# Kernel tuning notes

Measured on AMD Instinct MI355X. Metric: run time of the kernel, lower is better.

## Reference

```python
import jax, jax.numpy as jnp
from jax import lax
import numpy as np

B, S, H, DIN, BIN, NH, NL = 32, 256, 256, 16, 2, 8, 3
DH = H // NH


def setup_inputs() -> dict:
    key = jax.random.key(0)
    it = iter(jax.random.split(key, 40))
    def nrm(shape, s=0.05):
        return jax.random.normal(next(it), shape, jnp.float32) * s
    return {
        "parts": jax.random.normal(next(it), (B, S, DIN), jnp.float32),
        "bin_info": jax.random.normal(next(it), (B, BIN), jnp.float32),
        "target": jax.random.randint(next(it), (B, S), 0, S, dtype=jnp.int32),
        "pe_W1": nrm((H // 2, DIN)), "pe_b1": jnp.zeros((H // 2,), jnp.float32),
        "pe_W2": nrm((H // 2, H // 2)), "pe_b2": jnp.zeros((H // 2,), jnp.float32),
        "be_W1": nrm((H // 4, BIN)), "be_b1": jnp.zeros((H // 4,), jnp.float32),
        "be_W2": nrm((H // 4, H // 4)), "be_b2": jnp.zeros((H // 4,), jnp.float32),
        "pos_emb": nrm((S, H // 4)),
        "tr_Wqkv": nrm((NL, 3 * H, H)), "tr_bqkv": jnp.zeros((NL, 3 * H), jnp.float32),
        "tr_Wo": nrm((NL, H, H)), "tr_bo": jnp.zeros((NL, H), jnp.float32),
        "tr_ln1_g": jnp.ones((NL, H), jnp.float32), "tr_ln1_b": jnp.zeros((NL, H), jnp.float32),
        "tr_ff_W1": nrm((NL, 2 * H, H)), "tr_ff_b1": jnp.zeros((NL, 2 * H), jnp.float32),
        "tr_ff_W2": nrm((NL, H, 2 * H)), "tr_ff_b2": jnp.zeros((NL, H), jnp.float32),
        "tr_ln2_g": jnp.ones((NL, H), jnp.float32), "tr_ln2_b": jnp.zeros((NL, H), jnp.float32),
        "lstm_Wih": nrm((4 * H, H)), "lstm_Whh": nrm((4 * H, H)),
        "lstm_bih": jnp.zeros((4 * H,), jnp.float32), "lstm_bhh": jnp.zeros((4 * H,), jnp.float32),
        "ptr_W": nrm((H, H)), "ptr_b": jnp.zeros((H,), jnp.float32),
        "ptr_v": nrm((H,)),
    }


def _ln(x, g, b):
    m = x.mean(-1, keepdims=True)
    v = ((x - m) ** 2).mean(-1, keepdims=True)
    return (x - m) / jnp.sqrt(v + 1e-5) * g + b


def _forward(parts, bin_info, target, pe_W1, pe_b1, pe_W2, pe_b2,
             be_W1, be_b1, be_W2, be_b2, pos_emb,
             tr_Wqkv, tr_bqkv, tr_Wo, tr_bo, tr_ln1_g, tr_ln1_b,
             tr_ff_W1, tr_ff_b1, tr_ff_W2, tr_ff_b2, tr_ln2_g, tr_ln2_b,
             lstm_Wih, lstm_Whh, lstm_bih, lstm_bhh, ptr_W, ptr_b, ptr_v):
    # --- encode_inputs (dropout inactive in eval) ---
    p = jax.nn.relu(parts @ pe_W1.T + pe_b1) @ pe_W2.T + pe_b2            # [B,S,H/2]
    bb = jax.nn.relu(bin_info @ be_W1.T + be_b1) @ be_W2.T + be_b2        # [B,H/4]
    bb = jnp.broadcast_to(bb[:, None, :], (B, S, H // 4))
    pe = jnp.broadcast_to(pos_emb[None], (B, S, H // 4))
    x = jnp.concatenate([p, bb, pe], axis=-1)                             # [B,S,H]
    scale = 1.0 / np.sqrt(DH)
    for l in range(NL):  # post-norm TransformerEncoderLayer, relu FFN
        qkv = x @ tr_Wqkv[l].T + tr_bqkv[l]
        q, k, v = jnp.split(qkv, 3, axis=-1)
        q = q.reshape(B, S, NH, DH).transpose(0, 2, 1, 3)
        k = k.reshape(B, S, NH, DH).transpose(0, 2, 1, 3)
        v = v.reshape(B, S, NH, DH).transpose(0, 2, 1, 3)
        a = jax.nn.softmax(jnp.einsum('bhqd,bhkd->bhqk', q, k) * scale, axis=-1)
        o = jnp.einsum('bhqk,bhkd->bhqd', a, v).transpose(0, 2, 1, 3).reshape(B, S, H)
        x = _ln(x + o @ tr_Wo[l].T + tr_bo[l], tr_ln1_g[l], tr_ln1_b[l])
        ff = jax.nn.relu(x @ tr_ff_W1[l].T + tr_ff_b1[l]) @ tr_ff_W2[l].T + tr_ff_b2[l]
        x = _ln(x + ff, tr_ln2_g[l], tr_ln2_b[l])
    enc = x
    # Note: the original's inner MultiheadAttention calls never feed the
    # returned step_logits (part_logit is overwritten), so the faithful output is
    # logits[b,t,i] = v . tanh(ptr(h_t) + ptr(enc_i)), vectorized over i here.
    e_proj = enc @ ptr_W.T + ptr_b                                        # [B,S,H]
    bidx = jnp.arange(B)

    def step(carry, tgt_t):
        h, c, xin = carry
        g = xin @ lstm_Wih.T + lstm_bih + h @ lstm_Whh.T + lstm_bhh
        i, f, gg, o = jnp.split(g, 4, axis=-1)
        c = jax.nn.sigmoid(f) * c + jax.nn.sigmoid(i) * jnp.tanh(gg)
        h = jax.nn.sigmoid(o) * jnp.tanh(c)
        hp = h @ ptr_W.T + ptr_b                                          # [B,H]
        logits = jnp.tanh(hp[:, None, :] + e_proj) @ ptr_v                # [B,S]
        nxt = enc[bidx, tgt_t]                                            # teacher forcing
        return (h, c, nxt), logits

    z = jnp.zeros((B, H), jnp.float32)
    _, logits = lax.scan(step, (z, z, z), target.T)                       # [S,B,S]
    return logits.transpose(1, 0, 2)                                      # [B,S,S]


def reference(parts, bin_info, target, pe_W1, pe_b1, pe_W2, pe_b2,
              be_W1, be_b1, be_W2, be_b2, pos_emb,
              tr_Wqkv, tr_bqkv, tr_Wo, tr_bo, tr_ln1_g, tr_ln1_b,
              tr_ff_W1, tr_ff_b1, tr_ff_W2, tr_ff_b2, tr_ln2_g, tr_ln2_b,
              lstm_Wih, lstm_Whh, lstm_bih, lstm_bhh, ptr_W, ptr_b, ptr_v):
    return _forward(parts, bin_info, target, pe_W1, pe_b1, pe_W2, pe_b2,
                    be_W1, be_b1, be_W2, be_b2, pos_emb,
                    tr_Wqkv, tr_bqkv, tr_Wo, tr_bo, tr_ln1_g, tr_ln1_b,
                    tr_ff_W1, tr_ff_b1, tr_ff_W2, tr_ff_b2, tr_ln2_g, tr_ln2_b,
                    lstm_Wih, lstm_Whh, lstm_bih, lstm_bhh, ptr_W, ptr_b, ptr_v)
```

## Files before the change

kernel.cpp:

```cpp
#include <hip/hip_runtime.h>
#include <cstddef>

#define DEV __device__ __forceinline__

DEV float fexp2(float x) { return __builtin_amdgcn_exp2f(x); }
DEV float frcp(float x)  { return __builtin_amdgcn_rcpf(x); }
DEV float fsigm(float x) { return frcp(1.0f + fexp2(-1.44269504f * x)); }
DEV float ftanh_(float x){ return 1.0f - 2.0f * frcp(1.0f + fexp2(2.88539008f * x)); }

typedef _Float16 h2t __attribute__((ext_vector_type(2)));
typedef _Float16 v8h __attribute__((ext_vector_type(8)));
typedef float v4f __attribute__((ext_vector_type(4)));
union U32H2 { unsigned int u; h2t h; };
DEV h2t u2h(unsigned int u) { U32H2 x; x.u = u; return x.h; }

template <int BM, int BN, bool RELU, bool OUTF16>
__global__ __launch_bounds__(256) void hgemm_kernel(
    const _Float16* __restrict__ A, const _Float16* __restrict__ W,
    const float* __restrict__ bias1, const float* __restrict__ bias2,
    void* __restrict__ Cout, int M, int N, int K)
{
    constexpr int MT = BM / 32;
    constexpr int NT = BN / 32;
    constexpr int RA = BM / 64;
    constexpr int RB = BN / 64;
    __shared__ _Float16 As[BM * 32];
    __shared__ _Float16 Bs[BN * 32];

    const int tid = threadIdx.x;
    const int lane = tid & 63;
    const int lm = lane & 15, lq = lane >> 4;
    const int wrow = ((tid >> 6) & 1) * (BM / 2);
    const int wcol = (tid >> 7) * (BN / 2);
    const int m0 = blockIdx.x * BM, n0 = blockIdx.y * BN;
    const _Float16* Ab = A + (size_t)m0 * K;
    const _Float16* Wb = W + (size_t)n0 * K;

    v4f acc[MT][NT];
#pragma unroll
    for (int i = 0; i < MT; ++i)
#pragma unroll
        for (int j = 0; j < NT; ++j) acc[i][j] = (v4f){0.f, 0.f, 0.f, 0.f};

    const int rowS = tid >> 2, qS = tid & 3;

    uint4 ra[RA], rb[RB];
#pragma unroll
    for (int r = 0; r < RA; ++r)
        ra[r] = *(const uint4*)(Ab + (size_t)(rowS + 64 * r) * K + qS * 8);
#pragma unroll
    for (int r = 0; r < RB; ++r)
        rb[r] = *(const uint4*)(Wb + (size_t)(rowS + 64 * r) * K + qS * 8);

    for (int k0 = 0; k0 < K; k0 += 32) {
        __syncthreads();
#pragma unroll
        for (int r = 0; r < RA; ++r)
            *(uint4*)(As + (size_t)(tid + 256 * r) * 8) = ra[r];
#pragma unroll
        for (int r = 0; r < RB; ++r)
            *(uint4*)(Bs + (size_t)(tid + 256 * r) * 8) = rb[r];
        __syncthreads();
        int kn = k0 + 32;
        if (kn < K) {
#pragma unroll
            for (int r = 0; r < RA; ++r)
                ra[r] = *(const uint4*)(Ab + (size_t)(rowS + 64 * r) * K + kn + qS * 8);
#pragma unroll
            for (int r = 0; r < RB; ++r)
                rb[r] = *(const uint4*)(Wb + (size_t)(rowS + 64 * r) * K + kn + qS * 8);
        }
        v8h af[MT], bf[NT];
#pragma unroll
        for (int i = 0; i < MT; ++i)
            af[i] = *(const v8h*)(As + (size_t)(wrow + i * 16 + lm) * 32 + lq * 8);
#pragma unroll
        for (int j = 0; j < NT; ++j)
            bf[j] = *(const v8h*)(Bs + (size_t)(wcol + j * 16 + lm) * 32 + lq * 8);
#pragma unroll
        for (int i = 0; i < MT; ++i)
#pragma unroll
            for (int j = 0; j < NT; ++j)
                acc[i][j] = __builtin_amdgcn_mfma_f32_16x16x32_f16(
                    af[i], bf[j], acc[i][j], 0, 0, 0);
    }

#pragma unroll
    for (int j = 0; j < NT; ++j) {
        int col = n0 + wcol + j * 16 + lm;
        float bv = bias1[col];
        if (bias2) bv += bias2[col];
#pragma unroll
        for (int i = 0; i < MT; ++i) {
            int rbase = m0 + wrow + i * 16 + lq * 4;
#pragma unroll
            for (int rg = 0; rg < 4; ++rg) {
                float vv = acc[i][j][rg] + bv;
                if (RELU) vv = fmaxf(vv, 0.f);
                if (OUTF16)
                    ((_Float16*)Cout)[(size_t)(rbase + rg) * N + col] = (_Float16)vv;
                else
                    ((float*)Cout)[(size_t)(rbase + rg) * N + col] = vv;
            }
        }
    }
}

__global__ __launch_bounds__(256) void hgemm_ln_kernel(
    const _Float16* __restrict__ A, const _Float16* __restrict__ W,
    const float* __restrict__ bias, const float* __restrict__ gamma,
    const float* __restrict__ beta, float* __restrict__ X,
    _Float16* __restrict__ X16, int K)
{
    constexpr int BM = 64, BN = 256, MT = 2, NT = 8, RA = 1, RB = 4;
    __shared__ _Float16 As[BM * 32];
    __shared__ _Float16 Bs[BN * 32];
    __shared__ float redS[2][BM][2];

    const int tid = threadIdx.x;
    const int lane = tid & 63;
    const int lm = lane & 15, lq = lane >> 4;
    const int wrow = ((tid >> 6) & 1) * 32;
    const int wcol = (tid >> 7) * 128;
    const int half = tid >> 7;
    const int m0 = blockIdx.x * BM;
    const _Float16* Ab = A + (size_t)m0 * K;

    v4f acc[MT][NT];
#pragma unroll
    for (int i = 0; i < MT; ++i)
#pragma unroll
        for (int j = 0; j < NT; ++j) acc[i][j] = (v4f){0.f, 0.f, 0.f, 0.f};

    const int rowS = tid >> 2, qS = tid & 3;

    uint4 ra[RA], rb[RB];
#pragma unroll
    for (int r = 0; r < RA; ++r)
        ra[r] = *(const uint4*)(Ab + (size_t)(rowS + 64 * r) * K + qS * 8);
#pragma unroll
    for (int r = 0; r < RB; ++r)
        rb[r] = *(const uint4*)(W + (size_t)(rowS + 64 * r) * K + qS * 8);

    for (int k0 = 0; k0 < K; k0 += 32) {
        __syncthreads();
#pragma unroll
        for (int r = 0; r < RA; ++r)
            *(uint4*)(As + (size_t)(tid + 256 * r) * 8) = ra[r];
#pragma unroll
        for (int r = 0; r < RB; ++r)
            *(uint4*)(Bs + (size_t)(tid + 256 * r) * 8) = rb[r];
        __syncthreads();
        int kn = k0 + 32;
        if (kn < K) {
#pragma unroll
            for (int r = 0; r < RA; ++r)
                ra[r] = *(const uint4*)(Ab + (size_t)(rowS + 64 * r) * K + kn + qS * 8);
#pragma unroll
            for (int r = 0; r < RB; ++r)
                rb[r] = *(const uint4*)(W + (size_t)(rowS + 64 * r) * K + kn + qS * 8);
        }
        v8h af[MT], bf[NT];
#pragma unroll
        for (int i = 0; i < MT; ++i)
            af[i] = *(const v8h*)(As + (size_t)(wrow + i * 16 + lm) * 32 + lq * 8);
#pragma unroll
        for (int j = 0; j < NT; ++j)
            bf[j] = *(const v8h*)(Bs + (size_t)(wcol + j * 16 + lm) * 32 + lq * 8);
#pragma unroll
        for (int i = 0; i < MT; ++i)
#pragma unroll
            for (int j = 0; j < NT; ++j)
                acc[i][j] = __builtin_amdgcn_mfma_f32_16x16x32_f16(
                    af[i], bf[j], acc[i][j], 0, 0, 0);
    }

    float s[MT][4], s2[MT][4];
#pragma unroll
    for (int i = 0; i < MT; ++i)
#pragma unroll
        for (int rg = 0; rg < 4; ++rg) { s[i][rg] = 0.f; s2[i][rg] = 0.f; }
#pragma unroll
    for (int j = 0; j < NT; ++j) {
        int col = wcol + j * 16 + lm;
        float bv = bias[col];
#pragma unroll
        for (int i = 0; i < MT; ++i) {
            int rbase = m0 + wrow + i * 16 + lq * 4;
#pragma unroll
            for (int rg = 0; rg < 4; ++rg) {
                float y = acc[i][j][rg] + bv + X[(size_t)(rbase + rg) * 256 + col];
                acc[i][j][rg] = y;
                s[i][rg] += y;
                s2[i][rg] += y * y;
            }
        }
    }
#pragma unroll
    for (int i = 0; i < MT; ++i)
#pragma unroll
        for (int rg = 0; rg < 4; ++rg) {
            float a = s[i][rg], b2 = s2[i][rg];
#pragma unroll
            for (int m = 1; m < 16; m <<= 1) {
                a += __shfl_xor(a, m);
                b2 += __shfl_xor(b2, m);
            }
            if (lm == 0) {
                int rloc = wrow + i * 16 + lq * 4 + rg;
                redS[half][rloc][0] = a;
                redS[half][rloc][1] = b2;
            }
        }
    __syncthreads();
#pragma unroll
    for (int i = 0; i < MT; ++i) {
#pragma unroll
        for (int rg = 0; rg < 4; ++rg) {
            int rloc = wrow + i * 16 + lq * 4 + rg;
            float st = redS[0][rloc][0] + redS[1][rloc][0];
            float s2t = redS[0][rloc][1] + redS[1][rloc][1];
            float mean = st * (1.f / 256.f);
            float var = s2t * (1.f / 256.f) - mean * mean;
            float inv = rsqrtf(var + 1e-5f);
            size_t rowb = (size_t)(m0 + rloc) * 256;
#pragma unroll
            for (int j = 0; j < NT; ++j) {
                int col = wcol + j * 16 + lm;
                float o = (acc[i][j][rg] - mean) * inv * gamma[col] + beta[col];
                X[rowb + col] = o;
                X16[rowb + col] = (_Float16)o;
            }
        }
    }
}

__global__ __launch_bounds__(256) void cvt_fused_kernel(
    const float* __restrict__ s0, const float* __restrict__ s1,
    const float* __restrict__ s2, const float* __restrict__ s3,
    const float* __restrict__ s4, const float* __restrict__ s5,
    _Float16* __restrict__ dst,
    const float* __restrict__ Whh, unsigned int* __restrict__ WB,
    const float* __restrict__ bih, const float* __restrict__ bhh,
    float* __restrict__ PB)
{
    if (blockIdx.x < 7424) {
        int i = blockIdx.x * 256 + threadIdx.x;
        if (i >= 1900544) return;
        float val;
        if (i < 589824)       val = s0[i];
        else if (i < 786432)  val = s1[i - 589824];
        else if (i < 1179648) val = s2[i - 786432];
        else if (i < 1572864) val = s3[i - 1179648];
        else if (i < 1835008) {
            int idx = i - 1572864;
            int rp = idx >> 8, k = idx & 255;
            int j = rp >> 2, g = rp & 3;
            val = s4[(g * 256 + j) * 256 + k];
        }
        else                  val = s5[i - 1835008];
        dst[i] = (_Float16)val;
    } else {
        int idx = (blockIdx.x - 7424) * 256 + threadIdx.x;
        if (idx < 1024) {
            int j = idx >> 2, g = idx & 3;
            PB[idx] = bih[g * 256 + j] + bhh[g * 256 + j];
        }
        int l = idx & 3;
        int gt = idx >> 2;
        int tid = gt & 511;
        int q = gt >> 9;
        int i, c;
        if (q < 8)       { i = q >> 1; c = q & 1; }
        else if (q < 52) { int qq = q - 8; i = qq / 11; c = 2 + qq % 11; }
        else if (q < 56) { i = q - 52; c = 13; }
        else if (q < 58) { i = q - 56; c = 14; }
        else if (q < 60) { i = 2 + (q - 58); c = 14; }
        else             { i = q - 60; c = 15; }
        int r = ((tid & 255) << 2) + i;
        int k = ((tid >> 8) << 7) + (c << 3) + (l << 1);
        _Float16 lo = (_Float16)Whh[r * 256 + k];
        _Float16 hi = (_Float16)Whh[r * 256 + k + 1];
        U32H2 x; x.h = h2t{lo, hi};
        WB[idx] = x.u;
    }
}

__global__ __launch_bounds__(128) void part_enc_kernel(
    const float* __restrict__ parts, const float* __restrict__ W1,
    const float* __restrict__ b1, const float* __restrict__ W2,
    const float* __restrict__ b2, const float* __restrict__ bin_info,
    const float* __restrict__ be_W1, const float* __restrict__ be_b1,
    const float* __restrict__ be_W2, const float* __restrict__ be_b2,
    const float* __restrict__ pos_emb, float* __restrict__ X,
    _Float16* __restrict__ X16)
{
    __shared__ float W2s[128][129];
    __shared__ float h1[128];
    __shared__ float pin[16];
    __shared__ float h1b[64];
    __shared__ float bb_s[64];
    int tid = threadIdx.x;
    int b = blockIdx.x >> 3, s0 = (blockIdx.x & 7) * 32;
    for (int l = 0; l < 128; ++l) W2s[l][tid] = W2[l * 128 + tid];
    {
        float x0 = bin_info[b * 2], x1 = bin_info[b * 2 + 1];
        if (tid < 64)
            h1b[tid] = fmaxf(be_W1[tid * 2] * x0 + be_W1[tid * 2 + 1] * x1
                             + be_b1[tid], 0.f);
        __syncthreads();
        if (tid < 64) {
            float a = be_b2[tid];
#pragma unroll 4
            for (int e = 0; e < 64; ++e) a += be_W2[tid * 64 + e] * h1b[e];
            bb_s[tid] = a;
        }
        __syncthreads();
    }
    float w1r[16];
#pragma unroll
    for (int k = 0; k < 16; ++k) w1r[k] = W1[tid * 16 + k];
    float bias1v = b1[tid], bias2v = b2[tid];
    for (int si = 0; si < 32; ++si) {
        int s = s0 + si;
        size_t row = (size_t)b * 256 + s;
        if (tid < 16) pin[tid] = parts[row * 16 + tid];
        __syncthreads();
        float h = bias1v;
#pragma unroll
        for (int k = 0; k < 16; ++k) h += w1r[k] * pin[k];
        h1[tid] = fmaxf(h, 0.f);
        __syncthreads();
        float acc = bias2v;
#pragma unroll 4
        for (int e = 0; e < 128; ++e) acc += W2s[tid][e] * h1[e];
        X[row * 256 + tid] = acc;
        X16[row * 256 + tid] = (_Float16)acc;
        if (tid < 64) {
            float bbv = bb_s[tid];
            float pev = pos_emb[s * 64 + tid];
            X[row * 256 + 128 + tid] = bbv;
            X[row * 256 + 192 + tid] = pev;
            X16[row * 256 + 128 + tid] = (_Float16)bbv;
            X16[row * 256 + 192 + tid] = (_Float16)pev;
        }
        __syncthreads();
    }
}

__global__ __launch_bounds__(256) void attn_mfma_kernel(
    const _Float16* __restrict__ QKV, _Float16* __restrict__ O16)
{
    int bh = blockIdx.x;
    int b = bh >> 3, h = bh & 7;
    const int tid = threadIdx.x;
    const int w = tid >> 6;
    const int lane = tid & 63;
    const int lm = lane & 15, lq = lane >> 4;
    const float c_se = 0.17677669529663687f * 1.44269504f;

    __shared__ _Float16 Ks[4][256][8];
    __shared__ _Float16 Vt[32][264];
    __shared__ _Float16 Ps[4][16][264];

    const _Float16* qkvb = QKV + (size_t)(b * 256) * 768 + h * 32;
    {
        int s = tid;
        const _Float16* kr = qkvb + (size_t)s * 768 + 256;
#pragma unroll
        for (int c = 0; c < 4; ++c)
            *(uint4*)&Ks[c][s][0] = *(const uint4*)(kr + c * 8);
        const _Float16* vr = qkvb + (size_t)s * 768 + 512;
        _Float16 vtmp[32];
        *(uint4*)&vtmp[0]  = *(const uint4*)(vr);
        *(uint4*)&vtmp[8]  = *(const uint4*)(vr + 8);
        *(uint4*)&vtmp[16] = *(const uint4*)(vr + 16);
        *(uint4*)&vtmp[24] = *(const uint4*)(vr + 24);
#pragma unroll
        for (int d = 0; d < 32; ++d) Vt[d][s] = vtmp[d];
    }
    __syncthreads();

#pragma unroll 1
    for (int st = 0; st < 4; ++st) {
        int rt = w * 4 + st;
        v8h qf = *(const v8h*)(QKV + (size_t)(b * 256 + rt * 16 + lm) * 768
                               + h * 32 + lq * 8);
        v4f acc[16];
#pragma unroll
        for (int ct = 0; ct < 16; ++ct) {
            v8h kf = *(const v8h*)&Ks[lq][ct * 16 + lm][0];
            acc[ct] = __builtin_amdgcn_mfma_f32_16x16x32_f16(
                qf, kf, (v4f){0.f, 0.f, 0.f, 0.f}, 0, 0, 0);
        }
        float sminv[4];
#pragma unroll
        for (int r = 0; r < 4; ++r) {
            float m = acc[0][r];
#pragma unroll
            for (int ct = 1; ct < 16; ++ct) m = fmaxf(m, acc[ct][r]);
#pragma unroll
            for (int msk = 1; msk < 16; msk <<= 1)
                m = fmaxf(m, __shfl_xor(m, msk));
            float ssum = 0.f;
#pragma unroll
            for (int ct = 0; ct < 16; ++ct) {
                float e = fexp2((acc[ct][r] - m) * c_se);
                acc[ct][r] = e;
                ssum += e;
            }
#pragma unroll
            for (int msk = 1; msk < 16; msk <<= 1)
                ssum += __shfl_xor(ssum, msk);
            sminv[r] = frcp(ssum);
        }
#pragma unroll
        for (int ct = 0; ct < 16; ++ct)
#pragma unroll
            for (int r = 0; r < 4; ++r)
                Ps[w][lq * 4 + r][ct * 16 + lm] =
                    (_Float16)(acc[ct][r] * sminv[r]);
#pragma unroll
        for (int dt = 0; dt < 2; ++dt) {
            v4f o = (v4f){0.f, 0.f, 0.f, 0.f};
#pragma unroll
            for (int jc = 0; jc < 8; ++jc) {
                v8h pf = *(const v8h*)&Ps[w][lm][jc * 32 + lq * 8];
                v8h vf = *(const v8h*)&Vt[dt * 16 + lm][jc * 32 + lq * 8];
                o = __builtin_amdgcn_mfma_f32_16x16x32_f16(pf, vf, o, 0, 0, 0);
            }
#pragma unroll
            for (int r = 0; r < 4; ++r)
                O16[(size_t)(b * 256 + rt * 16 + lq * 4 + r) * 256
                    + h * 32 + dt * 16 + lm] = (_Float16)o[r];
        }
    }
}

__global__ __launch_bounds__(256) void gather_kernel(
    const float* __restrict__ X, const int* __restrict__ target,
    _Float16* __restrict__ Xg16)
{
    int row = blockIdx.x;
    int b = row >> 8, t = row & 255;
    int d = threadIdx.x;
    float val = 0.f;
    if (t > 0) {
        int src = target[b * 256 + t - 1];
        val = X[((size_t)b * 256 + src) * 256 + d];
    }
    Xg16[(size_t)row * 256 + d] = (_Float16)val;
}

__global__ __launch_bounds__(512) void lstm_kernel(
    const _Float16* __restrict__ g_in, const uint4* __restrict__ WB4,
    _Float16* __restrict__ HALL16)
{
    const int b = blockIdx.x;
    const int tid = threadIdx.x;
    const int kh = tid >> 8, j4 = tid & 255;

    __shared__ uint4 WL4[7168];
    __shared__ float gpart[2][1024];
    __shared__ uint4 h2v[32];
    unsigned int* h2_s = (unsigned int*)h2v;

#pragma unroll
    for (int g = 0; g < 14; ++g) {
        int src = (g < 8) ? g : (44 + g);
        WL4[g * 512 + tid] = WB4[src * 512 + tid];
    }
    uint4 wr[44];
#pragma unroll
    for (int q = 0; q < 44; ++q) wr[q] = WB4[(8 + q) * 512 + tid];
    if (tid < 128) h2_s[tid] = 0u;

    const _Float16* ginb = g_in + (size_t)b * 256 * 1024;
    uint2 gi = make_uint2(0u, 0u);
    if (tid < 256) gi = *(const uint2*)(ginb + tid * 4);
    float c_state = 0.f;
    const uint4* SW4 = WB4 + 58 * 512;
    __syncthreads();

    for (int t = 0; t < 256; ++t) {
        uint4 sw[6];
#pragma unroll
        for (int q = 0; q < 6; ++q) sw[q] = SW4[q * 512 + tid];

        float acc[4] = {0.f, 0.f, 0.f, 0.f};
#pragma unroll
        for (int c = 0; c < 16; ++c) {
            uint4 h4 = h2v[(kh << 4) + c];
            h2t hx = u2h(h4.x), hy = u2h(h4.y), hz = u2h(h4.z), hw = u2h(h4.w);
#pragma unroll
            for (int i = 0; i < 4; ++i) {
                uint4 w;
                if (c < 2)        w = WL4[((i << 1) + c) * 512 + tid];
                else if (c < 13)  w = wr[i * 11 + (c - 2)];
                else if (c == 13) w = WL4[(8 + i) * 512 + tid];
                else if (c == 14) w = (i < 2) ? WL4[(12 + i) * 512 + tid]
                                              : sw[i - 2];
                else              w = sw[2 + i];
                acc[i] = __builtin_amdgcn_fdot2(u2h(w.x), hx, acc[i], false);
                acc[i] = __builtin_amdgcn_fdot2(u2h(w.y), hy, acc[i], false);
                acc[i] = __builtin_amdgcn_fdot2(u2h(w.z), hz, acc[i], false);
                acc[i] = __builtin_amdgcn_fdot2(u2h(w.w), hw, acc[i], false);
            }
        }
        *(float4*)&gpart[kh][j4 << 2] = make_float4(acc[0], acc[1], acc[2], acc[3]);
        __syncthreads();

        if (tid < 256) {
            int j = tid;
            h2t p0 = u2h(gi.x), p1 = u2h(gi.y);
            float ig = (float)p0.x + gpart[0][j]       + gpart[1][j];
            float fg = (float)p0.y + gpart[0][j + 256] + gpart[1][j + 256];
            float gg = (float)p1.x + gpart[0][j + 512] + gpart[1][j + 512];
            float og = (float)p1.y + gpart[0][j + 768] + gpart[1][j + 768];
            c_state = fsigm(fg) * c_state + fsigm(ig) * ftanh_(gg);
            float h = fsigm(og) * ftanh_(c_state);
            HALL16[((size_t)(b * 256 + t)) * 256 + j] = (_Float16)h;
            U32H2 hxp; hxp.h = h2t{(_Float16)h, (_Float16)0.f};
            unsigned int hu = hxp.u & 0xffffu;
            unsigned int other = (unsigned int)__shfl_xor((int)hu, 1);
            if ((j & 1) == 0) h2_s[j >> 1] = hu | (other << 16);
            int tn = (t < 255) ? (t + 1) : 255;
            gi = *(const uint2*)(ginb + (size_t)tn * 1024 + j * 4);
        }
        __syncthreads();
    }
}

__global__ __launch_bounds__(256) void pointer_kernel(
    const float* __restrict__ HP, const float* __restrict__ EP,
    const float* __restrict__ v, float* __restrict__ out)
{
    int b = blockIdx.z, tt = blockIdx.y, it = blockIdx.x;
    __shared__ float hp_s[16][260];
    __shared__ float ep_s[16][260];
    __shared__ float v_s[256];
    __shared__ float red[4];
    int tid = threadIdx.x;
    const float cs = 2.88539008f;
    const float* hpb = HP + ((size_t)b * 256 + tt * 16) * 256;
    const float* epb = EP + ((size_t)b * 256 + it * 16) * 256;
#pragma unroll
    for (int l = 0; l < 4; ++l) {
        int idx = tid + l * 256;
        int r = idx >> 6, c4 = idx & 63;
        float4 hv = *(const float4*)(hpb + r * 256 + c4 * 4);
        hv.x *= cs; hv.y *= cs; hv.z *= cs; hv.w *= cs;
        *(float4*)&hp_s[r][c4 * 4] = hv;
        float4 ev = *(const float4*)(epb + r * 256 + c4 * 4);
        ev.x *= cs; ev.y *= cs; ev.z *= cs; ev.w *= cs;
        *(float4*)&ep_s[r][c4 * 4] = ev;
    }
    float vv = v[tid];
    v_s[tid] = vv;
    float vp = vv;
#pragma unroll
    for (int m = 1; m < 64; m <<= 1) vp += __shfl_xor(vp, m);
    if ((tid & 63) == 0) red[tid >> 6] = vp;
    __syncthreads();
    float vsum = red[0] + red[1] + red[2] + red[3];
    int tl = tid >> 4, il = tid & 15;
    float acc = 0.f;
#pragma unroll 4
    for (int d = 0; d < 256; ++d) {
        float sval = hp_s[tl][d] + ep_s[il][d];
        float r = frcp(1.0f + fexp2(sval));
        acc = fmaf(v_s[d], r, acc);
    }
    out[((size_t)b * 256 + tt * 16 + tl) * 256 + it * 16 + il] =
        vsum - 2.0f * acc;
}

extern "C" void kernel_launch(void* const* d_in, const int* in_sizes, int n_in,
                              void* d_out, int out_size, void* d_ws, size_t ws_size,
                              hipStream_t stream)
{
    const float* parts    = (const float*)d_in[0];
    const float* bin_info = (const float*)d_in[1];
    const int*   target   = (const int*)d_in[2];
    const float* pe_W1 = (const float*)d_in[3];
    const float* pe_b1 = (const float*)d_in[4];
    const float* pe_W2 = (const float*)d_in[5];
    const float* pe_b2 = (const float*)d_in[6];
    const float* be_W1 = (const float*)d_in[7];
    const float* be_b1 = (const float*)d_in[8];
    const float* be_W2 = (const float*)d_in[9];
    const float* be_b2 = (const float*)d_in[10];
    const float* pos_emb = (const float*)d_in[11];
    const float* tr_Wqkv = (const float*)d_in[12];
    const float* tr_bqkv = (const float*)d_in[13];
    const float* tr_Wo   = (const float*)d_in[14];
    const float* tr_bo   = (const float*)d_in[15];
    const float* tr_ln1_g = (const float*)d_in[16];
    const float* tr_ln1_b = (const float*)d_in[17];
    const float* tr_ff_W1 = (const float*)d_in[18];
    const float* tr_ff_b1 = (const float*)d_in[19];
    const float* tr_ff_W2 = (const float*)d_in[20];
    const float* tr_ff_b2 = (const float*)d_in[21];
    const float* tr_ln2_g = (const float*)d_in[22];
    const float* tr_ln2_b = (const float*)d_in[23];
    const float* lstm_Wih = (const float*)d_in[24];
    const float* lstm_Whh = (const float*)d_in[25];
    const float* lstm_bih = (const float*)d_in[26];
    const float* lstm_bhh = (const float*)d_in[27];
    const float* ptr_W = (const float*)d_in[28];
    const float* ptr_b = (const float*)d_in[29];
    const float* ptr_v = (const float*)d_in[30];

    float* ws = (float*)d_ws;
    float* X     = ws;
    float* S1    = X + 2097152;
    float* CF32  = S1 + 8388608;
    float* EPROJ = CF32 + 2097152;
    float* X16f  = EPROJ + 2097152;
    float* S2f   = X16f + 1048576;
    float* W16f  = S2f + 1048576;
    float* WBf   = W16f + 1048576;
    float* BBuf  = WBf + 131072;
    float* PB    = BBuf + 2048;

    _Float16* X16    = (_Float16*)X16f;
    _Float16* Xg16   = X16;
    _Float16* S2h    = (_Float16*)S2f;
    _Float16* HALL16 = S2h;
    _Float16* S1h    = (_Float16*)S1;
    _Float16* W16    = (_Float16*)W16f;
    _Float16* Wqkv16 = W16;
    _Float16* Wo16   = Wqkv16 + 589824;
    _Float16* Wff116 = Wo16 + 196608;
    _Float16* Wff216 = Wff116 + 393216;
    _Float16* Wih16  = Wff216 + 393216;
    _Float16* WpW16  = Wih16 + 262144;

    cvt_fused_kernel<<<7936, 256, 0, stream>>>(
        tr_Wqkv, tr_Wo, tr_ff_W1, tr_ff_W2, lstm_Wih, ptr_W, W16,
        lstm_Whh, (unsigned int*)WBf, lstm_bih, lstm_bhh, PB);

    part_enc_kernel<<<256, 128, 0, stream>>>(parts, pe_W1, pe_b1, pe_W2, pe_b2,
                                             bin_info, be_W1, be_b1, be_W2, be_b2,
                                             pos_emb, X, X16);

    for (int l = 0; l < 3; ++l) {
        hgemm_kernel<64, 128, false, true><<<dim3(128, 6), 256, 0, stream>>>(
            X16, Wqkv16 + (size_t)l * 196608, tr_bqkv + l * 768, nullptr,
            S1h, 8192, 768, 256);
        attn_mfma_kernel<<<256, 256, 0, stream>>>(S1h, S2h);
        hgemm_ln_kernel<<<128, 256, 0, stream>>>(
            S2h, Wo16 + (size_t)l * 65536, tr_bo + l * 256,
            tr_ln1_g + l * 256, tr_ln1_b + l * 256, X, X16, 256);
        hgemm_kernel<64, 128, true, true><<<dim3(128, 4), 256, 0, stream>>>(
            X16, Wff116 + (size_t)l * 131072, tr_ff_b1 + l * 512, nullptr,
            S1h, 8192, 512, 256);
        hgemm_ln_kernel<<<128, 256, 0, stream>>>(
            S1h, Wff216 + (size_t)l * 131072, tr_ff_b2 + l * 256,
            tr_ln2_g + l * 256, tr_ln2_b + l * 256, X, X16, 512);
    }

    hgemm_kernel<64, 64, false, false><<<dim3(128, 4), 256, 0, stream>>>(
        X16, WpW16, ptr_b, nullptr, EPROJ, 8192, 256, 256);
    gather_kernel<<<8192, 256, 0, stream>>>(X, target, Xg16);
    hgemm_kernel<64, 128, false, true><<<dim3(128, 8), 256, 0, stream>>>(
        Xg16, Wih16, PB, nullptr, S1h, 8192, 1024, 256);
    lstm_kernel<<<32, 512, 0, stream>>>(S1h, (const uint4*)WBf, HALL16);
    hgemm_kernel<64, 64, false, false><<<dim3(128, 4), 256, 0, stream>>>(
        HALL16, WpW16, ptr_b, nullptr, CF32, 8192, 256, 256);
    pointer_kernel<<<dim3(16, 16, 32), 256, 0, stream>>>(CF32, EPROJ, ptr_v,
                                                         (float*)d_out);
}
```

Before: 1.121 ms.

## Stream more LSTM recurrent weights from global, broadcast h via readlane

Shrinks the LSTM weight copy held in shared memory from 14 to 8 slabs, so 12 slabs per step (up from 6) are streamed from global/L2. The later loads are staggered inside the reduction loop so they overlap the dot products. The hidden state is now loaded once per lane as a single word and broadcast to the wave with readlane instead of vector LDS reads. This cuts LDS traffic and footprint, possibly enabling more occupancy, at the cost of more global load bandwidth per timestep and more register pressure.

```diff
diff --git a/kernel.cpp b/kernel.cpp
--- a/kernel.cpp
+++ b/kernel.cpp
@@ -273,10 +273,7 @@
         int i, c;
         if (q < 8)       { i = q >> 1; c = q & 1; }
         else if (q < 52) { int qq = q - 8; i = qq / 11; c = 2 + qq % 11; }
-        else if (q < 56) { i = q - 52; c = 13; }
-        else if (q < 58) { i = q - 56; c = 14; }
-        else if (q < 60) { i = 2 + (q - 58); c = 14; }
-        else             { i = q - 60; c = 15; }
+        else             { int qq = q - 52; c = 13 + (qq >> 2); i = qq & 3; }
         int r = ((tid & 255) << 2) + i;
         int k = ((tid >> 8) << 7) + (c << 3) + (l << 1);
         _Float16 lo = (_Float16)Whh[r * 256 + k];
@@ -460,16 +457,13 @@
     const int tid = threadIdx.x;
     const int kh = tid >> 8, j4 = tid & 255;
 
-    __shared__ uint4 WL4[7168];
+    __shared__ uint4 WL4[4096];
     __shared__ float gpart[2][1024];
     __shared__ uint4 h2v[32];
     unsigned int* h2_s = (unsigned int*)h2v;
 
 #pragma unroll
-    for (int g = 0; g < 14; ++g) {
-        int src = (g < 8) ? g : (44 + g);
-        WL4[g * 512 + tid] = WB4[src * 512 + tid];
-    }
+    for (int g = 0; g < 8; ++g) WL4[g * 512 + tid] = WB4[g * 512 + tid];
     uint4 wr[44];
 #pragma unroll
     for (int q = 0; q < 44; ++q) wr[q] = WB4[(8 + q) * 512 + tid];
@@ -479,28 +473,36 @@
     uint2 gi = make_uint2(0u, 0u);
     if (tid < 256) gi = *(const uint2*)(ginb + tid * 4);
     float c_state = 0.f;
-    const uint4* SW4 = WB4 + 58 * 512;
+    const uint4* SW4 = WB4 + 52 * 512;
     __syncthreads();
 
     for (int t = 0; t < 256; ++t) {
-        uint4 sw[6];
-#pragma unroll
-        for (int q = 0; q < 6; ++q) sw[q] = SW4[q * 512 + tid];
+        uint4 sw[12];
+#pragma unroll
+        for (int q = 0; q < 4; ++q) sw[q] = SW4[q * 512 + tid];
+
+        unsigned int hword = h2_s[(kh << 6) + (tid & 63)];
 
         float acc[4] = {0.f, 0.f, 0.f, 0.f};
 #pragma unroll
         for (int c = 0; c < 16; ++c) {
-            uint4 h4 = h2v[(kh << 4) + c];
-            h2t hx = u2h(h4.x), hy = u2h(h4.y), hz = u2h(h4.z), hw = u2h(h4.w);
+            if (c == 2) {
+#pragma unroll
+                for (int q = 4; q < 8; ++q) sw[q] = SW4[q * 512 + tid];
+            }
+            if (c == 6) {
+#pragma unroll
+                for (int q = 8; q < 12; ++q) sw[q] = SW4[q * 512 + tid];
+            }
+            h2t hx = u2h((unsigned int)__builtin_amdgcn_readlane((int)hword, 4 * c + 0));
+            h2t hy = u2h((unsigned int)__builtin_amdgcn_readlane((int)hword, 4 * c + 1));
+            h2t hz = u2h((unsigned int)__builtin_amdgcn_readlane((int)hword, 4 * c + 2));
+            h2t hw = u2h((unsigned int)__builtin_amdgcn_readlane((int)hword, 4 * c + 3));
 #pragma unroll
             for (int i = 0; i < 4; ++i) {
-                uint4 w;
-                if (c < 2)        w = WL4[((i << 1) + c) * 512 + tid];
-                else if (c < 13)  w = wr[i * 11 + (c - 2)];
-                else if (c == 13) w = WL4[(8 + i) * 512 + tid];
-                else if (c == 14) w = (i < 2) ? WL4[(12 + i) * 512 + tid]
-                                              : sw[i - 2];
-                else              w = sw[2 + i];
+                uint4 w = (c < 2)  ? WL4[((i << 1) + c) * 512 + tid]
+                        : (c < 13) ? wr[i * 11 + (c - 2)]
+                                   : sw[((c - 13) << 2) + i];
                 acc[i] = __builtin_amdgcn_fdot2(u2h(w.x), hx, acc[i], false);
                 acc[i] = __builtin_amdgcn_fdot2(u2h(w.y), hy, acc[i], false);
                 acc[i] = __builtin_amdgcn_fdot2(u2h(w.z), hz, acc[i], false);
```

After: 1.177 ms. 5.0% more time.
